# Optimization experiments

Hardware: AMD Instinct MI355X
Metric: run time of the kernel (lower is better)

The kernel has to match this reference:

```python
import jax, jax.numpy as jnp
from jax import lax
import numpy as np


def setup_inputs() -> dict:
    key = jax.random.key(0)
    x = jax.random.normal(key, (16, 1, 1536, 1536), dtype=jnp.float32)
    weight = jnp.ones((1, 1, 3, 3), dtype=jnp.float32) / 9.0
    return {"x": x, "weight": weight}


def _box3x3(z, weight):
    # z: (N, 1, H, W); zero padding=1 (torch conv2d default pad mode)
    return lax.conv_general_dilated(
        z, weight, window_strides=(1, 1), padding=((1, 1), (1, 1)),
        dimension_numbers=("NCHW", "OIHW", "NCHW"))


def _eig2x2(Axx, Axy, Ayy):
    # closed-form eigendecomposition of [[Axx, Axy], [Axy, Ayy]]
    T = Axx + Ayy
    D = Axx * Ayy - Axy * Axy
    s = jnp.sqrt(jnp.abs(T * T * 0.25 - D))
    l1 = T * 0.5 + s
    l2 = T * 0.5 - s
    e11 = l1 - Ayy
    e12 = Axy
    e21 = l2 - Ayy
    e22 = Axy
    small = jnp.abs(Axy) < 1e-9
    e11 = jnp.where(small, 1.0, e11)
    e12 = jnpp_zero = jnp.where(small, 0.0, e12)
    e21 = jnp.where(small, 0.0, e21)
    e22 = jnp.where(small, 1.0, e22)
    # sort so that the eigenvalue with smaller magnitude comes first
    lt = jnp.abs(l1) < jnp.abs(l2)
    lambda1 = jnp.where(lt, l1, l2)
    lambda2 = jnp.where(lt, l2, l1)
    e11_ = jnp.where(lt, e11, e21)
    e12_ = jnp.where(lt, e12, e22)
    e21_ = jnp.where(lt, e21, e11)
    e22_ = jnp.where(lt, e22, e12)
    # NOTE: original torch code has a typo (`labmda2_`), so only lambda1 gets ReLU
    lambda1 = jax.nn.relu(lambda1)
    return lambda1, lambda2, e11_, e12_, e21_, e22_


def reference(x, weight):
    n, c, h, w = x.shape
    # gx[..., 0] = x[..., 1] - x[..., 0]; gx[..., j] = x[..., j-1] - x[..., j]
    gx = jnp.concatenate([x[:, :, :, 1:2], x[:, :, :, :-1]], axis=3) - x
    gy = jnp.concatenate([x[:, :, 1:2, :], x[:, :, :-1, :]], axis=2) - x
    # per-channel box filter then mean over channels (c == 1 here)
    def smooth(z):
        zf = z.reshape(n * c, 1, h, w)
        out = _box3x3(zf, weight).reshape(n, c, h, w)
        return jnp.mean(out, axis=1)  # (N, H, W)
    Axx = smooth(gx * gx)
    Axy = smooth(gx * gy)
    Ayy = smooth(gy * gy)
    return _eig2x2(Axx, Axy, Ayy)
```

## Files before the change

### kernel.cpp

```cpp
#include <hip/hip_runtime.h>


typedef float f32x4 __attribute__((ext_vector_type(4)));
typedef float f32x2 __attribute__((ext_vector_type(2)));

constexpr int N_ = 16, H = 1536, W = 1536;

__global__ __launch_bounds__(256, 4)
void lsa_kernel(const float* __restrict__ x, float* __restrict__ out) {
    const int tid  = threadIdx.x;
    const int rsub = tid >> 6;
    const int csub = tid & 63;
    const int ti0  = blockIdx.y * 4;
    const int tj0  = blockIdx.x * 256;
    const int n    = blockIdx.z;
    const int p0   = ti0 + rsub;
    const int q0   = tj0 + 4 * csub;

    const size_t HW = (size_t)H * W;
    const size_t PLANE = (size_t)N_ * HW;
    const float* __restrict__ xn = x + (size_t)n * HW;

    float Sxx[6], Sxy[6], Syy[6];
    const bool interior = (p0 >= 2) & (p0 <= H - 2) & (q0 >= 2) & (q0 <= W - 6);

    if (interior) {
        float xv[4][8];
        const float* rp = xn + (size_t)(p0 - 2) * W + (q0 - 2);
#pragma unroll
        for (int d = 0; d < 4; ++d) {
            const f32x2 a = *reinterpret_cast<const f32x2*>(rp);
            const f32x4 b = *reinterpret_cast<const f32x4*>(rp + 2);
            const f32x2 c = *reinterpret_cast<const f32x2*>(rp + 6);
            xv[d][0] = a.x; xv[d][1] = a.y;
            xv[d][2] = b.x; xv[d][3] = b.y; xv[d][4] = b.z; xv[d][5] = b.w;
            xv[d][6] = c.x; xv[d][7] = c.y;
            rp += W;
        }
#pragma unroll
        for (int m = 0; m < 6; ++m) {
            float sxx = 0.f, sxy = 0.f, syy = 0.f;
#pragma unroll
            for (int d = 0; d < 3; ++d) {
                const float xc = xv[d + 1][m + 1];
                const float xl = xv[d + 1][m];
                const float xu = xv[d][m + 1];
                const float gx = xl - xc;
                const float gy = xu - xc;
                sxx = fmaf(gx, gx, sxx);
                sxy = fmaf(gx, gy, sxy);
                syy = fmaf(gy, gy, syy);
            }
            Sxx[m] = sxx; Sxy[m] = sxy; Syy[m] = syy;
        }
    } else {
#pragma unroll
        for (int m = 0; m < 6; ++m) {
            const int q = q0 - 1 + m;
            float sxx = 0.f, sxy = 0.f, syy = 0.f;
            if (q >= 0 && q < W) {
#pragma unroll
                for (int d = 0; d < 3; ++d) {
                    const int p = p0 - 1 + d;
                    if (p >= 0 && p < H) {
                        const float* prow = xn + (size_t)p * W;
                        const float xc = prow[q];
                        const float xl = (q == 0) ? prow[1] : prow[q - 1];
                        const float xu = (p == 0) ? xn[(size_t)W + q] : prow[q - W];
                        const float gx = xl - xc;
                        const float gy = xu - xc;
                        sxx = fmaf(gx, gx, sxx);
                        sxy = fmaf(gx, gy, sxy);
                        syy = fmaf(gy, gy, syy);
                    }
                }
            }
            Sxx[m] = sxx; Sxy[m] = sxy; Syy[m] = syy;
        }
    }

    f32x4 o_l1, o_l2, o_e11, o_e12, o_e21, o_e22;
    const float inv9 = 1.0f / 9.0f;
#pragma unroll
    for (int k = 0; k < 4; ++k) {
        const float Axx = (Sxx[k] + Sxx[k + 1] + Sxx[k + 2]) * inv9;
        const float Axy = (Sxy[k] + Sxy[k + 1] + Sxy[k + 2]) * inv9;
        const float Ayy = (Syy[k] + Syy[k + 1] + Syy[k + 2]) * inv9;

        const float T  = Axx + Ayy;
        const float Dd = Axx * Ayy - Axy * Axy;
        const float s  = sqrtf(fabsf(T * T * 0.25f - Dd));
        const float l1 = T * 0.5f + s;
        const float l2 = T * 0.5f - s;

        float e11 = l1 - Ayy, e12 = Axy;
        float e21 = l2 - Ayy, e22 = Axy;
        const bool small = fabsf(Axy) < 1e-9f;
        e11 = small ? 1.0f : e11;
        e12 = small ? 0.0f : e12;
        e21 = small ? 0.0f : e21;
        e22 = small ? 1.0f : e22;

        const bool lt = fabsf(l1) < fabsf(l2);
        o_l1[k]  = fmaxf(lt ? l1 : l2, 0.0f);
        o_l2[k]  = lt ? l2 : l1;
        o_e11[k] = lt ? e11 : e21;
        o_e12[k] = lt ? e12 : e22;
        o_e21[k] = lt ? e21 : e11;
        o_e22[k] = lt ? e22 : e12;
    }

    float* op = out + (size_t)n * HW + (size_t)p0 * W + q0;
    __builtin_nontemporal_store(o_l1,  reinterpret_cast<f32x4*>(op));
    __builtin_nontemporal_store(o_l2,  reinterpret_cast<f32x4*>(op + PLANE));
    __builtin_nontemporal_store(o_e11, reinterpret_cast<f32x4*>(op + 2 * PLANE));
    __builtin_nontemporal_store(o_e12, reinterpret_cast<f32x4*>(op + 3 * PLANE));
    __builtin_nontemporal_store(o_e21, reinterpret_cast<f32x4*>(op + 4 * PLANE));
    __builtin_nontemporal_store(o_e22, reinterpret_cast<f32x4*>(op + 5 * PLANE));
}

extern "C" void kernel_launch(void* const* d_in, const int* in_sizes, int n_in,
                              void* d_out, int out_size, void* d_ws, size_t ws_size,
                              hipStream_t stream) {
    const float* x = (const float*)d_in[0];
    float* out = (float*)d_out;

    dim3 grid(W / 256, H / 4, N_);
    dim3 block(256);
    lsa_kernel<<<grid, block, 0, stream>>>(x, out);
}
```

Measured before the change: 179.8 us.

## Compute two output rows per thread to share gradient products vertically

Each thread now produces two adjacent output rows, loading five input rows instead of four per row. The gradient products for the shared middle rows are computed once and added to both rows' vertical sums, which cuts redundant loads and arithmetic. The grid is halved in the row dimension. It also swaps sqrtf for the raw hardware sqrt builtin. In exchange, register pressure and per-thread latency rise, and the wave count halves.

```diff
diff --git a/kernel.cpp b/kernel.cpp
--- a/kernel.cpp
+++ b/kernel.cpp
@@ -6,90 +6,20 @@
 
 constexpr int N_ = 16, H = 1536, W = 1536;
 
-__global__ __launch_bounds__(256, 4)
-void lsa_kernel(const float* __restrict__ x, float* __restrict__ out) {
-    const int tid  = threadIdx.x;
-    const int rsub = tid >> 6;
-    const int csub = tid & 63;
-    const int ti0  = blockIdx.y * 4;
-    const int tj0  = blockIdx.x * 256;
-    const int n    = blockIdx.z;
-    const int p0   = ti0 + rsub;
-    const int q0   = tj0 + 4 * csub;
-
-    const size_t HW = (size_t)H * W;
-    const size_t PLANE = (size_t)N_ * HW;
-    const float* __restrict__ xn = x + (size_t)n * HW;
-
-    float Sxx[6], Sxy[6], Syy[6];
-    const bool interior = (p0 >= 2) & (p0 <= H - 2) & (q0 >= 2) & (q0 <= W - 6);
-
-    if (interior) {
-        float xv[4][8];
-        const float* rp = xn + (size_t)(p0 - 2) * W + (q0 - 2);
-#pragma unroll
-        for (int d = 0; d < 4; ++d) {
-            const f32x2 a = *reinterpret_cast<const f32x2*>(rp);
-            const f32x4 b = *reinterpret_cast<const f32x4*>(rp + 2);
-            const f32x2 c = *reinterpret_cast<const f32x2*>(rp + 6);
-            xv[d][0] = a.x; xv[d][1] = a.y;
-            xv[d][2] = b.x; xv[d][3] = b.y; xv[d][4] = b.z; xv[d][5] = b.w;
-            xv[d][6] = c.x; xv[d][7] = c.y;
-            rp += W;
-        }
-#pragma unroll
-        for (int m = 0; m < 6; ++m) {
-            float sxx = 0.f, sxy = 0.f, syy = 0.f;
-#pragma unroll
-            for (int d = 0; d < 3; ++d) {
-                const float xc = xv[d + 1][m + 1];
-                const float xl = xv[d + 1][m];
-                const float xu = xv[d][m + 1];
-                const float gx = xl - xc;
-                const float gy = xu - xc;
-                sxx = fmaf(gx, gx, sxx);
-                sxy = fmaf(gx, gy, sxy);
-                syy = fmaf(gy, gy, syy);
-            }
-            Sxx[m] = sxx; Sxy[m] = sxy; Syy[m] = syy;
-        }
-    } else {
-#pragma unroll
-        for (int m = 0; m < 6; ++m) {
-            const int q = q0 - 1 + m;
-            float sxx = 0.f, sxy = 0.f, syy = 0.f;
-            if (q >= 0 && q < W) {
-#pragma unroll
-                for (int d = 0; d < 3; ++d) {
-                    const int p = p0 - 1 + d;
-                    if (p >= 0 && p < H) {
-                        const float* prow = xn + (size_t)p * W;
-                        const float xc = prow[q];
-                        const float xl = (q == 0) ? prow[1] : prow[q - 1];
-                        const float xu = (p == 0) ? xn[(size_t)W + q] : prow[q - W];
-                        const float gx = xl - xc;
-                        const float gy = xu - xc;
-                        sxx = fmaf(gx, gx, sxx);
-                        sxy = fmaf(gx, gy, sxy);
-                        syy = fmaf(gy, gy, syy);
-                    }
-                }
-            }
-            Sxx[m] = sxx; Sxy[m] = sxy; Syy[m] = syy;
-        }
-    }
-
+__device__ __forceinline__ void eig_row(
+    const float S_xx[6], const float S_xy[6], const float S_yy[6],
+    float* __restrict__ op, size_t PLANE) {
     f32x4 o_l1, o_l2, o_e11, o_e12, o_e21, o_e22;
     const float inv9 = 1.0f / 9.0f;
 #pragma unroll
     for (int k = 0; k < 4; ++k) {
-        const float Axx = (Sxx[k] + Sxx[k + 1] + Sxx[k + 2]) * inv9;
-        const float Axy = (Sxy[k] + Sxy[k + 1] + Sxy[k + 2]) * inv9;
-        const float Ayy = (Syy[k] + Syy[k + 1] + Syy[k + 2]) * inv9;
+        const float Axx = (S_xx[k] + S_xx[k + 1] + S_xx[k + 2]) * inv9;
+        const float Axy = (S_xy[k] + S_xy[k + 1] + S_xy[k + 2]) * inv9;
+        const float Ayy = (S_yy[k] + S_yy[k + 1] + S_yy[k + 2]) * inv9;
 
         const float T  = Axx + Ayy;
         const float Dd = Axx * Ayy - Axy * Axy;
-        const float s  = sqrtf(fabsf(T * T * 0.25f - Dd));
+        const float s  = __builtin_amdgcn_sqrtf(fabsf(T * T * 0.25f - Dd));
         const float l1 = T * 0.5f + s;
         const float l2 = T * 0.5f - s;
 
@@ -109,8 +39,6 @@
         o_e21[k] = lt ? e21 : e11;
         o_e22[k] = lt ? e22 : e12;
     }
-
-    float* op = out + (size_t)n * HW + (size_t)p0 * W + q0;
     __builtin_nontemporal_store(o_l1,  reinterpret_cast<f32x4*>(op));
     __builtin_nontemporal_store(o_l2,  reinterpret_cast<f32x4*>(op + PLANE));
     __builtin_nontemporal_store(o_e11, reinterpret_cast<f32x4*>(op + 2 * PLANE));
@@ -119,13 +47,103 @@
     __builtin_nontemporal_store(o_e22, reinterpret_cast<f32x4*>(op + 5 * PLANE));
 }
 
+__global__ __launch_bounds__(256, 4)
+void lsa_kernel(const float* __restrict__ x, float* __restrict__ out) {
+    const int tid  = threadIdx.x;
+    const int rsub = tid >> 6;
+    const int csub = tid & 63;
+    const int P0   = blockIdx.y * 8 + 2 * rsub;
+    const int q0   = blockIdx.x * 256 + 4 * csub;
+    const int n    = blockIdx.z;
+
+    const size_t HW = (size_t)H * W;
+    const size_t PLANE = (size_t)N_ * HW;
+    const float* __restrict__ xn = x + (size_t)n * HW;
+
+    float S0xx[6], S0xy[6], S0yy[6];
+    float S1xx[6], S1xy[6], S1yy[6];
+
+    const bool interior = (P0 >= 2) & (P0 <= H - 3) & (q0 >= 2) & (q0 <= W - 6);
+
+    if (interior) {
+        float xv[5][8];
+        const float* rp = xn + (size_t)(P0 - 2) * W + (q0 - 2);
+#pragma unroll
+        for (int d = 0; d < 5; ++d) {
+            const f32x2 a = *reinterpret_cast<const f32x2*>(rp);
+            const f32x4 b = *reinterpret_cast<const f32x4*>(rp + 2);
+            const f32x2 c = *reinterpret_cast<const f32x2*>(rp + 6);
+            xv[d][0] = a.x; xv[d][1] = a.y;
+            xv[d][2] = b.x; xv[d][3] = b.y; xv[d][4] = b.z; xv[d][5] = b.w;
+            xv[d][6] = c.x; xv[d][7] = c.y;
+            rp += W;
+        }
+#pragma unroll
+        for (int m = 0; m < 6; ++m) {
+            S0xx[m] = 0.f; S0xy[m] = 0.f; S0yy[m] = 0.f;
+            S1xx[m] = 0.f; S1xy[m] = 0.f; S1yy[m] = 0.f;
+        }
+#pragma unroll
+        for (int t = 0; t < 4; ++t) {
+#pragma unroll
+            for (int m = 0; m < 6; ++m) {
+                const float xc = xv[t + 1][m + 1];
+                const float xl = xv[t + 1][m];
+                const float xu = xv[t][m + 1];
+                const float gx = xl - xc;
+                const float gy = xu - xc;
+                const float pxx = gx * gx;
+                const float pxy = gx * gy;
+                const float pyy = gy * gy;
+                if (t < 3) { S0xx[m] += pxx; S0xy[m] += pxy; S0yy[m] += pyy; }
+                if (t > 0) { S1xx[m] += pxx; S1xy[m] += pxy; S1yy[m] += pyy; }
+            }
+        }
+    } else {
+#pragma unroll
+        for (int r = 0; r < 2; ++r) {
+            float* Sxx = r ? S1xx : S0xx;
+            float* Sxy = r ? S1xy : S0xy;
+            float* Syy = r ? S1yy : S0yy;
+            const int pr = P0 + r;
+#pragma unroll
+            for (int m = 0; m < 6; ++m) {
+                const int q = q0 - 1 + m;
+                float sxx = 0.f, sxy = 0.f, syy = 0.f;
+                if (q >= 0 && q < W) {
+#pragma unroll
+                    for (int d = 0; d < 3; ++d) {
+                        const int p = pr - 1 + d;
+                        if (p >= 0 && p < H) {
+                            const float* prow = xn + (size_t)p * W;
+                            const float xc = prow[q];
+                            const float xl = (q == 0) ? prow[1] : prow[q - 1];
+                            const float xu = (p == 0) ? xn[(size_t)W + q] : prow[q - W];
+                            const float gx = xl - xc;
+                            const float gy = xu - xc;
+                            sxx = fmaf(gx, gx, sxx);
+                            sxy = fmaf(gx, gy, sxy);
+                            syy = fmaf(gy, gy, syy);
+                        }
+                    }
+                }
+                Sxx[m] = sxx; Sxy[m] = sxy; Syy[m] = syy;
+            }
+        }
+    }
+
+    float* op = out + (size_t)n * HW + (size_t)P0 * W + q0;
+    eig_row(S0xx, S0xy, S0yy, op, PLANE);
+    eig_row(S1xx, S1xy, S1yy, op + W, PLANE);
+}
+
 extern "C" void kernel_launch(void* const* d_in, const int* in_sizes, int n_in,
                               void* d_out, int out_size, void* d_ws, size_t ws_size,
                               hipStream_t stream) {
     const float* x = (const float*)d_in[0];
     float* out = (float*)d_out;
 
-    dim3 grid(W / 256, H / 4, N_);
+    dim3 grid(W / 256, H / 8, N_);
     dim3 block(256);
     lsa_kernel<<<grid, block, 0, stream>>>(x, out);
 }
```

Measured after the change: 171.7 us, median of 2. -4.5%, faster.
